# Performance work log

Measured on AMD Instinct MI355X. Metric: run time of the kernel, lower is better.

## Reference

```python
import jax, jax.numpy as jnp
import numpy as np

ROPE_BASE = 10000.0
NEG_INF = jnp.finfo(jnp.float32).min


def _rope(x, pos):
    # x: [B, L, H, D], pos: [L] absolute positions. Rotate-half RoPE.
    D = x.shape[-1]
    half = D // 2
    inv_freq = 1.0 / (ROPE_BASE ** (jnp.arange(half, dtype=jnp.float32) / half))
    ang = pos.astype(jnp.float32)[:, None] * inv_freq  # [L, half]
    cos = jnp.cos(ang)[None, :, None, :]
    sin = jnp.sin(ang)[None, :, None, :]
    x1, x2 = x[..., :half], x[..., half:]
    return jnp.concatenate([x1 * cos - x2 * sin, x1 * sin + x2 * cos], axis=-1)


def setup_inputs() -> dict:
    key = jax.random.key(0)
    kq, kk, kv = jax.random.split(key, 3)
    B, L, H, Dh = 4, 4096, 16, 64
    return {
        "q": jax.random.normal(kq, (B, L, H, Dh), dtype=jnp.float32),
        "k": jax.random.normal(kk, (B, L, H, Dh), dtype=jnp.float32),
        "v": jax.random.normal(kv, (B, L, H, Dh), dtype=jnp.float32),
        "chunk_size": 1024,
        "start_index": 0,
    }


def reference(q, k, v, chunk_size, start_index):
    B, L, H, Dh = q.shape
    Dv = v.shape[-1]
    C = chunk_size
    assert L % C == 0  # chosen shapes avoid padding; original pads otherwise
    n = L // C
    # Per-chunk RoPE with offset start_index + chunk_offset equals
    # full-sequence RoPE at absolute positions start_index + arange(L).
    pos = start_index + jnp.arange(L)
    q_rot = _rope(q.astype(jnp.float32), pos)
    k_rot = _rope(k.astype(jnp.float32), pos)
    qc = q_rot.reshape(B, n, C, H, Dh)
    kc = k_rot.reshape(B, n, C, H, Dh)
    vc = v.astype(jnp.float32).reshape(B, n, C, H, Dv)
    # Unscaled (scale=1.0) block-diagonal causal attention.
    scores = jnp.einsum("bnqhd,bnkhd->bnhqk", qc, kc)
    causal = jnp.tril(jnp.ones((C, C), dtype=jnp.bool_))
    scores = jnp.where(causal, scores, NEG_INF)
    attn = jax.nn.softmax(scores, axis=-1)
    attn = jnp.where(jnp.isnan(attn), 0.0, attn)
    out = jnp.einsum("bnhqk,bnkhd->bnqhd", attn, vc)
    return out.reshape(B, L, H, Dv).astype(q.dtype)
```

## Files before the change

kernel.cpp:

```cpp
#include <hip/hip_runtime.h>

typedef _Float16 f16x8 __attribute__((ext_vector_type(8)));
typedef _Float16 f16x4 __attribute__((ext_vector_type(4)));
typedef _Float16 f16x2 __attribute__((ext_vector_type(2)));
typedef float    f32x4 __attribute__((ext_vector_type(4)));

#define B_N    4
#define L_TOT  4096
#define H_N    16
#define DH     64
#define HALF_D 32
#define QT     64
#define KT     64
#define LDSP   72

#define LOG2_BASE 13.287712379549449f
#define LOG2E     1.4426950408889634f

#define TAB_BYTES  ((size_t)L_TOT * 64 * sizeof(float))
#define IMG_BYTES  ((size_t)B_N * H_N * 64 * 8192)

__global__ void rope_table_kernel(const int* __restrict__ sidx, float* __restrict__ tab) {
    int idx = blockIdx.x * 256 + (int)threadIdx.x;
    if (idx >= L_TOT * HALF_D) return;
    int l = idx >> 5;
    int j = idx & 31;
    float invf = exp2f(-(float)j * (LOG2_BASE / (float)HALF_D));
    float ang = (float)(sidx[0] + l) * invf;
    float s, c;
    sincosf(ang, &s, &c);
    tab[l * 64 + j] = c;
    tab[l * 64 + HALF_D + j] = s;
}

__global__ __launch_bounds__(256)
void prep_kernel(const float* __restrict__ k, const float* __restrict__ v,
                 const float* __restrict__ tab,
                 unsigned char* __restrict__ kimg, unsigned char* __restrict__ vimg)
{
    __shared__ float Vs[64][65];
    int bid = (int)blockIdx.x;
    int t = (int)threadIdx.x;

    if (bid < 4096) {
        int task = bid * 256 + t;
        int c = task & 3;
        int rowid = task >> 2;
        int l = rowid & (L_TOT - 1);
        int bh = rowid >> 12;
        int b = bh >> 4, h = bh & 15;
        int d0 = c * 8;
        const float* src = k + (((size_t)b * L_TOT + l) * H_N + h) * (size_t)DH;
        f32x4 x1a = *(const f32x4*)(src + d0);
        f32x4 x1b = *(const f32x4*)(src + d0 + 4);
        f32x4 x2a = *(const f32x4*)(src + d0 + HALF_D);
        f32x4 x2b = *(const f32x4*)(src + d0 + HALF_D + 4);
        const float* tr = tab + (size_t)l * 64 + d0;
        f32x4 ca = *(const f32x4*)(tr);
        f32x4 cb = *(const f32x4*)(tr + 4);
        f32x4 sa = *(const f32x4*)(tr + HALF_D);
        f32x4 sb = *(const f32x4*)(tr + HALF_D + 4);
        f16x8 olo, ohi;
#pragma unroll
        for (int j = 0; j < 4; ++j) {
            olo[j]     = (_Float16)(x1a[j] * ca[j] - x2a[j] * sa[j]);
            olo[j + 4] = (_Float16)(x1b[j] * cb[j] - x2b[j] * sb[j]);
            ohi[j]     = (_Float16)(x1a[j] * sa[j] + x2a[j] * ca[j]);
            ohi[j + 4] = (_Float16)(x1b[j] * sb[j] + x2b[j] * cb[j]);
        }
        size_t tile = (size_t)bh * 64 + (l >> 6);
        unsigned char* dst = kimg + tile * 8192 + (size_t)(l & 63) * 128;
        int sw = (c ^ (l & 7)) << 4;
        *(f16x8*)(dst + sw)        = olo;
        *(f16x8*)(dst + (sw ^ 64)) = ohi;
    } else {
        int vb = bid - 4096;
        int tile = vb & 63;
        int h = (vb >> 6) & 15;
        int b = vb >> 10;
        int kbase = tile * 64;
        int row = t >> 2, cb = t & 3;
        const float* src = v + (((size_t)b * L_TOT + kbase + row) * H_N + h) * (size_t)DH + cb * 16;
        f32x4 a0 = *(const f32x4*)(src);
        f32x4 a1 = *(const f32x4*)(src + 4);
        f32x4 a2 = *(const f32x4*)(src + 8);
        f32x4 a3 = *(const f32x4*)(src + 12);
#pragma unroll
        for (int j = 0; j < 4; ++j) {
            Vs[row][cb * 16 + j]      = a0[j];
            Vs[row][cb * 16 + 4 + j]  = a1[j];
            Vs[row][cb * 16 + 8 + j]  = a2[j];
            Vs[row][cb * 16 + 12 + j] = a3[j];
        }
        __syncthreads();
        size_t tbase = ((size_t)(b * 16 + h) * 64 + tile) * 8192;
#pragma unroll
        for (int e = 0; e < 2; ++e) {
            int task = e * 256 + t;
            int dv = task >> 3, c = task & 7;
            f16x8 o;
#pragma unroll
            for (int j = 0; j < 8; ++j) o[j] = (_Float16)Vs[8 * c + j][dv];
            *(f16x8*)(vimg + tbase + (size_t)dv * 128 + ((c ^ (dv & 7)) << 4)) = o;
        }
    }
}

__device__ __forceinline__ void gl_lds16(const void* g, void* lds) {
    __builtin_amdgcn_global_load_lds(
        (const __attribute__((address_space(1))) unsigned int*)g,
        (__attribute__((address_space(3))) unsigned int*)lds, 16, 0, 0);
}

__global__ __launch_bounds__(256, 4)
void attn_main_kernel(const float* __restrict__ q, const int* __restrict__ csz,
                      const float* __restrict__ tab,
                      const unsigned char* __restrict__ kimg,
                      const unsigned char* __restrict__ vimg,
                      float* __restrict__ out) {
    __shared__ __align__(16) unsigned char smem[40960];

    const int tid  = (int)threadIdx.x;
    const int lane = tid & 63;
    const int w    = tid >> 6;
    const int cl   = lane & 15;
    const int g    = lane >> 4;
    const int e7   = cl & 7;

    const int bid0  = (int)blockIdx.x;
    const int wg    = (bid0 & 7) * 512 + (bid0 >> 3);
    const int qx    = wg & 63;
    const int h     = (wg >> 6) & 15;
    const int b     = wg >> 10;

    const int C   = csz[0];
    const int tpc = C >> 6;
    const int qtile = qx ^ ((tpc - 1) & 63);
    const int kb0 = (qtile / tpc) * tpc;

    const int qr = qtile * QT + w * 16 + cl;
    const float* qs = q + (((size_t)b * L_TOT + qr) * H_N + h) * (size_t)DH;
    f32x4 x1a = *(const f32x4*)(qs + 8 * g);
    f32x4 x1b = *(const f32x4*)(qs + 8 * g + 4);
    f32x4 x2a = *(const f32x4*)(qs + 8 * g + HALF_D);
    f32x4 x2b = *(const f32x4*)(qs + 8 * g + HALF_D + 4);
    const float* tr = tab + (size_t)qr * 64 + 8 * g;
    f32x4 ca = *(const f32x4*)(tr);
    f32x4 cb = *(const f32x4*)(tr + 4);
    f32x4 sa = *(const f32x4*)(tr + HALF_D);
    f32x4 sb = *(const f32x4*)(tr + HALF_D + 4);
    f16x8 qa0, qa1;
#pragma unroll
    for (int j = 0; j < 4; ++j) {
        qa0[j]     = (_Float16)((x1a[j] * ca[j] - x2a[j] * sa[j]) * LOG2E);
        qa0[j + 4] = (_Float16)((x1b[j] * cb[j] - x2b[j] * sb[j]) * LOG2E);
        qa1[j]     = (_Float16)((x1a[j] * sa[j] + x2a[j] * ca[j]) * LOG2E);
        qa1[j + 4] = (_Float16)((x1b[j] * sb[j] + x2b[j] * cb[j]) * LOG2E);
    }

    const unsigned char* ksrc = kimg + (size_t)(b * 16 + h) * 64 * 8192;
    const unsigned char* vsrc = vimg + (size_t)(b * 16 + h) * 64 * 8192;

    const int krd = cl * 128 + ((g ^ e7) << 4);
    const int pwb = cl * 128 + (((g >> 1) ^ e7) << 4) + (g & 1) * 8;
    char* Pw = (char*)(smem + 32768 + w * 2048);

    f32x4 o[4] = {};
    float m = -3e38f, l = 0.f;

    {
        const unsigned char* gk = ksrc + (size_t)kb0 * 8192;
        const unsigned char* gv = vsrc + (size_t)kb0 * 8192;
        gl_lds16(gk + tid * 16,        smem + tid * 16);
        gl_lds16(gk + tid * 16 + 4096, smem + tid * 16 + 4096);
        gl_lds16(gv + tid * 16,        smem + 16384 + tid * 16);
        gl_lds16(gv + tid * 16 + 4096, smem + 16384 + tid * 16 + 4096);
    }

    int pb = 0;
    for (int kb = kb0; kb <= qtile; ++kb) {
        __syncthreads();

        const char* Kb = (const char*)(smem + pb * 8192);
        const char* Vb = (const char*)(smem + 16384 + pb * 8192);
        if (kb < qtile) {
            const unsigned char* nk = ksrc + (size_t)(kb + 1) * 8192;
            const unsigned char* nv = vsrc + (size_t)(kb + 1) * 8192;
            unsigned char* lk = smem + (pb ^ 1) * 8192;
            unsigned char* lv = smem + 16384 + (pb ^ 1) * 8192;
            gl_lds16(nk + tid * 16,        lk + tid * 16);
            gl_lds16(nk + tid * 16 + 4096, lk + tid * 16 + 4096);
            gl_lds16(nv + tid * 16,        lv + tid * 16);
            gl_lds16(nv + tid * 16 + 4096, lv + tid * 16 + 4096);
        }

        f32x4 sc[4];
        __builtin_amdgcn_s_setprio(1);
#pragma unroll
        for (int ct = 0; ct < 4; ++ct) {
            f16x8 kf0 = *(const f16x8*)(Kb + krd + ct * 2048);
            f16x8 kf1 = *(const f16x8*)(Kb + ((krd + ct * 2048) ^ 64));
            f32x4 z = {};
            z = __builtin_amdgcn_mfma_f32_16x16x32_f16(kf0, qa0, z, 0, 0, 0);
            sc[ct] = __builtin_amdgcn_mfma_f32_16x16x32_f16(kf1, qa1, z, 0, 0, 0);
        }
        __builtin_amdgcn_s_setprio(0);

        if (kb == qtile) {
            const int qloc = w * 16 + cl;
#pragma unroll
            for (int ct = 0; ct < 4; ++ct)
#pragma unroll
                for (int r = 0; r < 4; ++r)
                    if (ct * 16 + 4 * g + r > qloc) sc[ct][r] = -3e38f;
        }

        float mx = sc[0][0];
#pragma unroll
        for (int ct = 0; ct < 4; ++ct)
#pragma unroll
            for (int r = 0; r < 4; ++r) mx = fmaxf(mx, sc[ct][r]);
        mx = fmaxf(mx, __shfl_xor(mx, 16));
        mx = fmaxf(mx, __shfl_xor(mx, 32));
        if (__any(mx - m > 8.0f)) {
            float mn  = fmaxf(m, mx);
            float scl = exp2f(m - mn);
            m = mn;
            l *= scl;
#pragma unroll
            for (int ct = 0; ct < 4; ++ct)
#pragma unroll
                for (int r = 0; r < 4; ++r) o[ct][r] *= scl;
        }
        float ps = 0.f;
#pragma unroll
        for (int ct = 0; ct < 4; ++ct)
#pragma unroll
            for (int r = 0; r < 4; ++r) {
                float p = exp2f(sc[ct][r] - m);
                sc[ct][r] = p;
                ps += p;
            }
        ps += __shfl_xor(ps, 16);
        ps += __shfl_xor(ps, 32);
        l += ps;

#pragma unroll
        for (int c = 0; c < 4; ++c) {
            f16x2 lo = __builtin_bit_cast(f16x2, __builtin_amdgcn_cvt_pkrtz(sc[c][0], sc[c][1]));
            f16x2 hi = __builtin_bit_cast(f16x2, __builtin_amdgcn_cvt_pkrtz(sc[c][2], sc[c][3]));
            f16x4 pv = __builtin_shufflevector(lo, hi, 0, 1, 2, 3);
            *(f16x4*)(Pw + (pwb ^ (c << 5))) = pv;
        }

        f16x8 pa0 = *(const f16x8*)(Pw + krd);
        f16x8 pa1 = *(const f16x8*)(Pw + (krd ^ 64));
        __builtin_amdgcn_s_setprio(1);
#pragma unroll
        for (int ct = 0; ct < 4; ++ct) {
            f16x8 v0 = *(const f16x8*)(Vb + krd + ct * 2048);
            o[ct] = __builtin_amdgcn_mfma_f32_16x16x32_f16(v0, pa0, o[ct], 0, 0, 0);
        }
#pragma unroll
        for (int ct = 0; ct < 4; ++ct) {
            f16x8 v1 = *(const f16x8*)(Vb + ((krd + ct * 2048) ^ 64));
            o[ct] = __builtin_amdgcn_mfma_f32_16x16x32_f16(v1, pa1, o[ct], 0, 0, 0);
        }
        __builtin_amdgcn_s_setprio(0);

        pb ^= 1;
    }

    __syncthreads();
    float* Ow = (float*)smem;
    float inv = 1.f / l;
#pragma unroll
    for (int ct = 0; ct < 4; ++ct)
#pragma unroll
        for (int r = 0; r < 4; ++r)
            Ow[(w * 16 + cl) * 66 + ct * 16 + 4 * g + r] = o[ct][r] * inv;
    __syncthreads();
    int row_l = tid >> 2;
    int cb4 = (tid & 3) * 16;
    const float* orow = Ow + row_l * 66 + cb4;
    float* gdst = out + (((size_t)b * L_TOT + qtile * QT + row_l) * H_N + h) * (size_t)DH + cb4;
#pragma unroll
    for (int jj = 0; jj < 4; ++jj) {
        f32x4 val;
#pragma unroll
        for (int x = 0; x < 4; ++x) val[x] = orow[4 * jj + x];
        *(f32x4*)(gdst + 4 * jj) = val;
    }
}

__device__ __forceinline__ void rope_cs_inline(float pos, int d, float* cc, float* ss) {
    float invf = exp2f(-(float)d * (LOG2_BASE / (float)HALF_D));
    float s, c;
    sincosf(pos * invf, &s, &c);
    *cc = c;
    *ss = s;
}

template<bool TAB>
__global__ __launch_bounds__(256)
void chunked_attn_kernel(const float* __restrict__ q, const float* __restrict__ k,
                         const float* __restrict__ v, const int* __restrict__ csz,
                         const int* __restrict__ sidx, const float* __restrict__ tab,
                         float* __restrict__ out)
{
    __shared__ _Float16 Ks[KT][LDSP];
    __shared__ _Float16 Vt[DH][LDSP];
    __shared__ _Float16 Ps[4][16][LDSP];

    const int tid  = (int)threadIdx.x;
    const int lane = tid & 63;
    const int w    = tid >> 6;
    const int cl   = lane & 15;
    const int g    = lane >> 4;

    const int bid   = (int)blockIdx.x;
    const int qtile = bid & (L_TOT / QT - 1);
    const int h     = (bid >> 6) & (H_N - 1);
    const int b     = bid >> 10;

    const int C   = csz[0];
    const int S0  = sidx[0];
    const int tpc = C / KT;
    const int kb0 = (qtile / tpc) * tpc;

    const int qrow = qtile * QT + w * 16 + cl;
    const size_t qoff = (((size_t)b * L_TOT + qrow) * H_N + h) * (size_t)DH;
    f32x4 x1a = *(const f32x4*)(q + qoff + 8 * g);
    f32x4 x1b = *(const f32x4*)(q + qoff + 8 * g + 4);
    f32x4 x2a = *(const f32x4*)(q + qoff + 8 * g + HALF_D);
    f32x4 x2b = *(const f32x4*)(q + qoff + 8 * g + HALF_D + 4);
    f32x4 ca, cb, sa, sb;
    if (TAB) {
        const float* tr = tab + (size_t)qrow * 64 + 8 * g;
        ca = *(const f32x4*)(tr);
        cb = *(const f32x4*)(tr + 4);
        sa = *(const f32x4*)(tr + HALF_D);
        sb = *(const f32x4*)(tr + HALF_D + 4);
    } else {
        float pos = (float)(S0 + qrow);
#pragma unroll
        for (int j = 0; j < 4; ++j) {
            float c0, s0, c1, s1;
            rope_cs_inline(pos, 8 * g + j,     &c0, &s0);
            rope_cs_inline(pos, 8 * g + 4 + j, &c1, &s1);
            ca[j] = c0; sa[j] = s0;
            cb[j] = c1; sb[j] = s1;
        }
    }
    f16x8 qa0, qa1;
#pragma unroll
    for (int j = 0; j < 4; ++j) {
        qa0[j]     = (_Float16)(x1a[j] * ca[j] - x2a[j] * sa[j]);
        qa0[j + 4] = (_Float16)(x1b[j] * cb[j] - x2b[j] * sb[j]);
        qa1[j]     = (_Float16)(x1a[j] * sa[j] + x2a[j] * ca[j]);
        qa1[j + 4] = (_Float16)(x1b[j] * sb[j] + x2b[j] * cb[j]);
    }

    f32x4 o[4] = {};
    float m_r[4], l_r[4];
#pragma unroll
    for (int r = 0; r < 4; ++r) { m_r[r] = -3e38f; l_r[r] = 0.f; }

    for (int kb = kb0; kb <= qtile; ++kb) {
        __syncthreads();
        const int kbase = kb * KT;

#pragma unroll
        for (int e = 0; e < 2; ++e) {
            int task = e * 256 + tid;
            int kk = task >> 3;
            int dg = (task & 7) * 4;
            int grow = kbase + kk;
            size_t off = (((size_t)b * L_TOT + grow) * H_N + h) * (size_t)DH;
            f32x4 x1 = *(const f32x4*)(k + off + dg);
            f32x4 x2 = *(const f32x4*)(k + off + dg + HALF_D);
            f32x4 cc, ss;
            if (TAB) {
                const float* tr2 = tab + (size_t)grow * 64 + dg;
                cc = *(const f32x4*)(tr2);
                ss = *(const f32x4*)(tr2 + HALF_D);
            } else {
                float pos = (float)(S0 + grow);
#pragma unroll
                for (int j = 0; j < 4; ++j) {
                    float c0, s0;
                    rope_cs_inline(pos, dg + j, &c0, &s0);
                    cc[j] = c0; ss[j] = s0;
                }
            }
            f16x4 o1, o2;
#pragma unroll
            for (int j = 0; j < 4; ++j) {
                o1[j] = (_Float16)(x1[j] * cc[j] - x2[j] * ss[j]);
                o2[j] = (_Float16)(x1[j] * ss[j] + x2[j] * cc[j]);
            }
            *(f16x4*)&Ks[kk][dg]          = o1;
            *(f16x4*)&Ks[kk][dg + HALF_D] = o2;
        }

#pragma unroll
        for (int e = 0; e < 4; ++e) {
            int task = e * 256 + tid;
            int kk = task >> 4;
            int dq = (task & 15) * 4;
            int grow = kbase + kk;
            size_t off = (((size_t)b * L_TOT + grow) * H_N + h) * (size_t)DH + dq;
            f32x4 x = *(const f32x4*)(v + off);
#pragma unroll
            for (int i = 0; i < 4; ++i) Vt[dq + i][kk] = (_Float16)x[i];
        }
        __syncthreads();

        f32x4 sc[4];
#pragma unroll
        for (int ct = 0; ct < 4; ++ct) {
            f16x8 kf0 = *(const f16x8*)&Ks[ct * 16 + cl][8 * g];
            f16x8 kf1 = *(const f16x8*)&Ks[ct * 16 + cl][8 * g + HALF_D];
            f32x4 z = {};
            z = __builtin_amdgcn_mfma_f32_16x16x32_f16(qa0, kf0, z, 0, 0, 0);
            sc[ct] = __builtin_amdgcn_mfma_f32_16x16x32_f16(qa1, kf1, z, 0, 0, 0);
        }

        const int rowt = w * 16 + 4 * g;
        if (kb == qtile) {
#pragma unroll
            for (int ct = 0; ct < 4; ++ct)
#pragma unroll
                for (int r = 0; r < 4; ++r)
                    if (ct * 16 + cl > rowt + r) sc[ct][r] = -3e38f;
        }

        f32x4 mt;
#pragma unroll
        for (int r = 0; r < 4; ++r)
            mt[r] = fmaxf(fmaxf(sc[0][r], sc[1][r]), fmaxf(sc[2][r], sc[3][r]));
#pragma unroll
        for (int off = 1; off < 16; off <<= 1) {
#pragma unroll
            for (int r = 0; r < 4; ++r)
                mt[r] = fmaxf(mt[r], __shfl_xor(mt[r], off));
        }
        float scale_r[4];
#pragma unroll
        for (int r = 0; r < 4; ++r) {
            float mn = fmaxf(m_r[r], mt[r]);
            scale_r[r] = __expf(m_r[r] - mn);
            m_r[r] = mn;
        }
        f32x4 psum = {};
#pragma unroll
        for (int ct = 0; ct < 4; ++ct) {
#pragma unroll
            for (int r = 0; r < 4; ++r) {
                float p = __expf(sc[ct][r] - m_r[r]);
                sc[ct][r] = p;
                psum[r] += p;
            }
        }
#pragma unroll
        for (int off = 1; off < 16; off <<= 1) {
#pragma unroll
            for (int r = 0; r < 4; ++r)
                psum[r] += __shfl_xor(psum[r], off);
        }
#pragma unroll
        for (int r = 0; r < 4; ++r) l_r[r] = l_r[r] * scale_r[r] + psum[r];
#pragma unroll
        for (int ct = 0; ct < 4; ++ct)
#pragma unroll
            for (int r = 0; r < 4; ++r) o[ct][r] *= scale_r[r];

#pragma unroll
        for (int ct = 0; ct < 4; ++ct)
#pragma unroll
            for (int r = 0; r < 4; ++r)
                Ps[w][4 * g + r][ct * 16 + cl] = (_Float16)sc[ct][r];

#pragma unroll
        for (int st = 0; st < 2; ++st) {
            f16x8 pa = *(const f16x8*)&Ps[w][cl][8 * g + 32 * st];
#pragma unroll
            for (int ct = 0; ct < 4; ++ct) {
                f16x8 vb = *(const f16x8*)&Vt[ct * 16 + cl][8 * g + 32 * st];
                o[ct] = __builtin_amdgcn_mfma_f32_16x16x32_f16(pa, vb, o[ct], 0, 0, 0);
            }
        }
    }

#pragma unroll
    for (int ct = 0; ct < 4; ++ct) {
#pragma unroll
        for (int r = 0; r < 4; ++r) {
            int row = qtile * QT + w * 16 + 4 * g + r;
            float val = o[ct][r] / l_r[r];
            out[(((size_t)b * L_TOT + row) * H_N + h) * (size_t)DH + ct * 16 + cl] = val;
        }
    }
}

extern "C" void kernel_launch(void* const* d_in, const int* in_sizes, int n_in,
                              void* d_out, int out_size, void* d_ws, size_t ws_size,
                              hipStream_t stream) {
    const float* q  = (const float*)d_in[0];
    const float* k  = (const float*)d_in[1];
    const float* v  = (const float*)d_in[2];
    const int* csz  = (const int*)d_in[3];
    const int* sidx = (const int*)d_in[4];
    float* out = (float*)d_out;

    const size_t TOTAL = TAB_BYTES + 2 * IMG_BYTES;
    const int grid = B_N * H_N * (L_TOT / QT);

    if (ws_size >= TOTAL) {
        float* tab = (float*)d_ws;
        unsigned char* kimg = (unsigned char*)d_ws + TAB_BYTES;
        unsigned char* vimg = kimg + IMG_BYTES;
        rope_table_kernel<<<(L_TOT * HALF_D + 255) / 256, 256, 0, stream>>>(sidx, tab);
        prep_kernel<<<8192, 256, 0, stream>>>(k, v, tab, kimg, vimg);
        attn_main_kernel<<<grid, 256, 0, stream>>>(q, csz, tab, kimg, vimg, out);
    } else if (ws_size >= TAB_BYTES) {
        float* tab = (float*)d_ws;
        rope_table_kernel<<<(L_TOT * HALF_D + 255) / 256, 256, 0, stream>>>(sidx, tab);
        chunked_attn_kernel<true><<<grid, 256, 0, stream>>>(q, k, v, csz, sidx, tab, out);
    } else {
        chunked_attn_kernel<false><<<grid, 256, 0, stream>>>(q, k, v, csz, sidx, nullptr, out);
    }
}
```

Measured before the change: 149.7 us.

## Read K/V fragments directly from global memory instead of LDS double-buffering

Drops the LDS double-buffered staging of K and V tiles (global_load_lds plus per-iteration barriers). Each wave now loads its MFMA fragments straight from the prepacked global images, and the XOR swizzle is removed from both the packing kernel and the readers. Shared memory shrinks to the P scratch and output staging, and launch bounds rise to 5 blocks per CU to raise occupancy. The cost is that each of the four waves fetches the same K/V tile from global/L2 separately, and there is no explicit prefetch overlap.

```diff
diff --git a/kernel.cpp b/kernel.cpp
--- a/kernel.cpp
+++ b/kernel.cpp
@@ -70,9 +70,8 @@
         }
         size_t tile = (size_t)bh * 64 + (l >> 6);
         unsigned char* dst = kimg + tile * 8192 + (size_t)(l & 63) * 128;
-        int sw = (c ^ (l & 7)) << 4;
-        *(f16x8*)(dst + sw)        = olo;
-        *(f16x8*)(dst + (sw ^ 64)) = ohi;
+        *(f16x8*)(dst + (c << 4))      = olo;
+        *(f16x8*)(dst + (c << 4) + 64) = ohi;
     } else {
         int vb = bid - 4096;
         int tile = vb & 63;
@@ -101,24 +100,18 @@
             f16x8 o;
 #pragma unroll
             for (int j = 0; j < 8; ++j) o[j] = (_Float16)Vs[8 * c + j][dv];
-            *(f16x8*)(vimg + tbase + (size_t)dv * 128 + ((c ^ (dv & 7)) << 4)) = o;
+            *(f16x8*)(vimg + tbase + (size_t)dv * 128 + (c << 4)) = o;
         }
     }
 }
 
-__device__ __forceinline__ void gl_lds16(const void* g, void* lds) {
-    __builtin_amdgcn_global_load_lds(
-        (const __attribute__((address_space(1))) unsigned int*)g,
-        (__attribute__((address_space(3))) unsigned int*)lds, 16, 0, 0);
-}
-
-__global__ __launch_bounds__(256, 4)
+__global__ __launch_bounds__(256, 5)
 void attn_main_kernel(const float* __restrict__ q, const int* __restrict__ csz,
                       const float* __restrict__ tab,
                       const unsigned char* __restrict__ kimg,
                       const unsigned char* __restrict__ vimg,
                       float* __restrict__ out) {
-    __shared__ __align__(16) unsigned char smem[40960];
+    __shared__ __align__(16) unsigned char smem[16896];
 
     const int tid  = (int)threadIdx.x;
     const int lane = tid & 63;
@@ -161,45 +154,24 @@
     const unsigned char* ksrc = kimg + (size_t)(b * 16 + h) * 64 * 8192;
     const unsigned char* vsrc = vimg + (size_t)(b * 16 + h) * 64 * 8192;
 
+    const int rln = cl * 128 + g * 16;
     const int krd = cl * 128 + ((g ^ e7) << 4);
     const int pwb = cl * 128 + (((g >> 1) ^ e7) << 4) + (g & 1) * 8;
-    char* Pw = (char*)(smem + 32768 + w * 2048);
+    char* Pw = (char*)(smem + w * 2048);
 
     f32x4 o[4] = {};
     float m = -3e38f, l = 0.f;
 
-    {
-        const unsigned char* gk = ksrc + (size_t)kb0 * 8192;
-        const unsigned char* gv = vsrc + (size_t)kb0 * 8192;
-        gl_lds16(gk + tid * 16,        smem + tid * 16);
-        gl_lds16(gk + tid * 16 + 4096, smem + tid * 16 + 4096);
-        gl_lds16(gv + tid * 16,        smem + 16384 + tid * 16);
-        gl_lds16(gv + tid * 16 + 4096, smem + 16384 + tid * 16 + 4096);
-    }
-
-    int pb = 0;
     for (int kb = kb0; kb <= qtile; ++kb) {
-        __syncthreads();
-
-        const char* Kb = (const char*)(smem + pb * 8192);
-        const char* Vb = (const char*)(smem + 16384 + pb * 8192);
-        if (kb < qtile) {
-            const unsigned char* nk = ksrc + (size_t)(kb + 1) * 8192;
-            const unsigned char* nv = vsrc + (size_t)(kb + 1) * 8192;
-            unsigned char* lk = smem + (pb ^ 1) * 8192;
-            unsigned char* lv = smem + 16384 + (pb ^ 1) * 8192;
-            gl_lds16(nk + tid * 16,        lk + tid * 16);
-            gl_lds16(nk + tid * 16 + 4096, lk + tid * 16 + 4096);
-            gl_lds16(nv + tid * 16,        lv + tid * 16);
-            gl_lds16(nv + tid * 16 + 4096, lv + tid * 16 + 4096);
-        }
+        const char* kt = (const char*)(ksrc + (size_t)kb * 8192);
+        const char* vt = (const char*)(vsrc + (size_t)kb * 8192);
 
         f32x4 sc[4];
         __builtin_amdgcn_s_setprio(1);
 #pragma unroll
         for (int ct = 0; ct < 4; ++ct) {
-            f16x8 kf0 = *(const f16x8*)(Kb + krd + ct * 2048);
-            f16x8 kf1 = *(const f16x8*)(Kb + ((krd + ct * 2048) ^ 64));
+            f16x8 kf0 = *(const f16x8*)(kt + rln + ct * 2048);
+            f16x8 kf1 = *(const f16x8*)(kt + rln + ct * 2048 + 64);
             f32x4 z = {};
             z = __builtin_amdgcn_mfma_f32_16x16x32_f16(kf0, qa0, z, 0, 0, 0);
             sc[ct] = __builtin_amdgcn_mfma_f32_16x16x32_f16(kf1, qa1, z, 0, 0, 0);
@@ -258,17 +230,15 @@
         __builtin_amdgcn_s_setprio(1);
 #pragma unroll
         for (int ct = 0; ct < 4; ++ct) {
-            f16x8 v0 = *(const f16x8*)(Vb + krd + ct * 2048);
+            f16x8 v0 = *(const f16x8*)(vt + rln + ct * 2048);
             o[ct] = __builtin_amdgcn_mfma_f32_16x16x32_f16(v0, pa0, o[ct], 0, 0, 0);
         }
 #pragma unroll
         for (int ct = 0; ct < 4; ++ct) {
-            f16x8 v1 = *(const f16x8*)(Vb + ((krd + ct * 2048) ^ 64));
+            f16x8 v1 = *(const f16x8*)(vt + rln + ct * 2048 + 64);
             o[ct] = __builtin_amdgcn_mfma_f32_16x16x32_f16(v1, pa1, o[ct], 0, 0, 0);
         }
         __builtin_amdgcn_s_setprio(0);
-
-        pb ^= 1;
     }
 
     __syncthreads();
```

After: 389.8 us. +160.4%, slower.

## Switch attention kernel to 32x32 MFMA with register-resident P and 2-wave blocks

Applied to the files above, without the earlier changes.

Rewrites the main attention kernel so each wave owns 32 query rows and uses 32x32x16 MFMA for both QK^T and PV. The softmax probabilities are packed to f16 and swapped between half-waves with lane shuffles instead of a round trip through LDS. The block shrinks to 128 threads, and outputs are written straight from registers without the LDS staging pass. This is meant to cut LDS traffic and instruction count per tile, at the cost of more accumulator registers and fewer waves per block to hide latency.

```diff
diff --git a/kernel.cpp b/kernel.cpp
--- a/kernel.cpp
+++ b/kernel.cpp
@@ -2,8 +2,8 @@
 
 typedef _Float16 f16x8 __attribute__((ext_vector_type(8)));
 typedef _Float16 f16x4 __attribute__((ext_vector_type(4)));
-typedef _Float16 f16x2 __attribute__((ext_vector_type(2)));
 typedef float    f32x4 __attribute__((ext_vector_type(4)));
+typedef float    f32x16 __attribute__((ext_vector_type(16)));
 
 #define B_N    4
 #define L_TOT  4096
@@ -112,25 +112,29 @@
         (__attribute__((address_space(3))) unsigned int*)lds, 16, 0, 0);
 }
 
-__global__ __launch_bounds__(256, 4)
+__device__ __forceinline__ unsigned pku(float a, float b) {
+    return __builtin_bit_cast(unsigned, __builtin_amdgcn_cvt_pkrtz(a, b));
+}
+
+__global__ __launch_bounds__(128, 2)
 void attn_main_kernel(const float* __restrict__ q, const int* __restrict__ csz,
                       const float* __restrict__ tab,
                       const unsigned char* __restrict__ kimg,
                       const unsigned char* __restrict__ vimg,
                       float* __restrict__ out) {
-    __shared__ __align__(16) unsigned char smem[40960];
+    __shared__ __align__(16) unsigned char smem[32768];
 
     const int tid  = (int)threadIdx.x;
     const int lane = tid & 63;
     const int w    = tid >> 6;
-    const int cl   = lane & 15;
-    const int g    = lane >> 4;
-    const int e7   = cl & 7;
+    const int qi   = lane & 31;
+    const int h    = lane >> 5;
+    const int e7   = lane & 7;
 
     const int bid0  = (int)blockIdx.x;
     const int wg    = (bid0 & 7) * 512 + (bid0 >> 3);
     const int qx    = wg & 63;
-    const int h     = (wg >> 6) & 15;
+    const int hh    = (wg >> 6) & 15;
     const int b     = wg >> 10;
 
     const int C   = csz[0];
@@ -138,43 +142,49 @@
     const int qtile = qx ^ ((tpc - 1) & 63);
     const int kb0 = (qtile / tpc) * tpc;
 
-    const int qr = qtile * QT + w * 16 + cl;
-    const float* qs = q + (((size_t)b * L_TOT + qr) * H_N + h) * (size_t)DH;
-    f32x4 x1a = *(const f32x4*)(qs + 8 * g);
-    f32x4 x1b = *(const f32x4*)(qs + 8 * g + 4);
-    f32x4 x2a = *(const f32x4*)(qs + 8 * g + HALF_D);
-    f32x4 x2b = *(const f32x4*)(qs + 8 * g + HALF_D + 4);
-    const float* tr = tab + (size_t)qr * 64 + 8 * g;
-    f32x4 ca = *(const f32x4*)(tr);
-    f32x4 cb = *(const f32x4*)(tr + 4);
-    f32x4 sa = *(const f32x4*)(tr + HALF_D);
-    f32x4 sb = *(const f32x4*)(tr + HALF_D + 4);
-    f16x8 qa0, qa1;
+    const int qg = qtile * QT + 32 * w + qi;
+    const int qloc = 32 * w + qi;
+
+    const float* qs = q + (((size_t)b * L_TOT + qg) * H_N + hh) * (size_t)DH;
+    const int d0 = 8 * h;
+    f32x4 xa0 = *(const f32x4*)(qs + d0);       f32x4 xa1 = *(const f32x4*)(qs + d0 + 4);
+    f32x4 xb0 = *(const f32x4*)(qs + d0 + 16);  f32x4 xb1 = *(const f32x4*)(qs + d0 + 20);
+    f32x4 xc0 = *(const f32x4*)(qs + d0 + 32);  f32x4 xc1 = *(const f32x4*)(qs + d0 + 36);
+    f32x4 xd0 = *(const f32x4*)(qs + d0 + 48);  f32x4 xd1 = *(const f32x4*)(qs + d0 + 52);
+    const float* tr = tab + (size_t)qg * 64;
+    f32x4 ca0 = *(const f32x4*)(tr + d0);       f32x4 ca1 = *(const f32x4*)(tr + d0 + 4);
+    f32x4 cb0 = *(const f32x4*)(tr + d0 + 16);  f32x4 cb1 = *(const f32x4*)(tr + d0 + 20);
+    f32x4 sa0 = *(const f32x4*)(tr + 32 + d0);      f32x4 sa1 = *(const f32x4*)(tr + 32 + d0 + 4);
+    f32x4 sb0 = *(const f32x4*)(tr + 32 + d0 + 16); f32x4 sb1 = *(const f32x4*)(tr + 32 + d0 + 20);
+    f16x8 qf0, qf1, qf2, qf3;
 #pragma unroll
     for (int j = 0; j < 4; ++j) {
-        qa0[j]     = (_Float16)((x1a[j] * ca[j] - x2a[j] * sa[j]) * LOG2E);
-        qa0[j + 4] = (_Float16)((x1b[j] * cb[j] - x2b[j] * sb[j]) * LOG2E);
-        qa1[j]     = (_Float16)((x1a[j] * sa[j] + x2a[j] * ca[j]) * LOG2E);
-        qa1[j + 4] = (_Float16)((x1b[j] * sb[j] + x2b[j] * cb[j]) * LOG2E);
-    }
-
-    const unsigned char* ksrc = kimg + (size_t)(b * 16 + h) * 64 * 8192;
-    const unsigned char* vsrc = vimg + (size_t)(b * 16 + h) * 64 * 8192;
-
-    const int krd = cl * 128 + ((g ^ e7) << 4);
-    const int pwb = cl * 128 + (((g >> 1) ^ e7) << 4) + (g & 1) * 8;
-    char* Pw = (char*)(smem + 32768 + w * 2048);
-
-    f32x4 o[4] = {};
+        qf0[j]     = (_Float16)((xa0[j] * ca0[j] - xc0[j] * sa0[j]) * LOG2E);
+        qf0[j + 4] = (_Float16)((xa1[j] * ca1[j] - xc1[j] * sa1[j]) * LOG2E);
+        qf1[j]     = (_Float16)((xb0[j] * cb0[j] - xd0[j] * sb0[j]) * LOG2E);
+        qf1[j + 4] = (_Float16)((xb1[j] * cb1[j] - xd1[j] * sb1[j]) * LOG2E);
+        qf2[j]     = (_Float16)((xa0[j] * sa0[j] + xc0[j] * ca0[j]) * LOG2E);
+        qf2[j + 4] = (_Float16)((xa1[j] * sa1[j] + xc1[j] * ca1[j]) * LOG2E);
+        qf3[j]     = (_Float16)((xb0[j] * sb0[j] + xd0[j] * cb0[j]) * LOG2E);
+        qf3[j + 4] = (_Float16)((xb1[j] * sb1[j] + xd1[j] * cb1[j]) * LOG2E);
+    }
+
+    const unsigned char* ksrc = kimg + (size_t)(b * 16 + hh) * 64 * 8192;
+    const unsigned char* vsrc = vimg + (size_t)(b * 16 + hh) * 64 * 8192;
+
+    const int rbase = qi * 128;
+
+    f32x16 acc0 = {}, acc1 = {};
     float m = -3e38f, l = 0.f;
 
     {
         const unsigned char* gk = ksrc + (size_t)kb0 * 8192;
         const unsigned char* gv = vsrc + (size_t)kb0 * 8192;
-        gl_lds16(gk + tid * 16,        smem + tid * 16);
-        gl_lds16(gk + tid * 16 + 4096, smem + tid * 16 + 4096);
-        gl_lds16(gv + tid * 16,        smem + 16384 + tid * 16);
-        gl_lds16(gv + tid * 16 + 4096, smem + 16384 + tid * 16 + 4096);
+#pragma unroll
+        for (int e = 0; e < 4; ++e) {
+            gl_lds16(gk + tid * 16 + e * 2048, smem + tid * 16 + e * 2048);
+            gl_lds16(gv + tid * 16 + e * 2048, smem + 16384 + tid * 16 + e * 2048);
+        }
     }
 
     int pb = 0;
@@ -188,39 +198,50 @@
             const unsigned char* nv = vsrc + (size_t)(kb + 1) * 8192;
             unsigned char* lk = smem + (pb ^ 1) * 8192;
             unsigned char* lv = smem + 16384 + (pb ^ 1) * 8192;
-            gl_lds16(nk + tid * 16,        lk + tid * 16);
-            gl_lds16(nk + tid * 16 + 4096, lk + tid * 16 + 4096);
-            gl_lds16(nv + tid * 16,        lv + tid * 16);
-            gl_lds16(nv + tid * 16 + 4096, lv + tid * 16 + 4096);
-        }
-
-        f32x4 sc[4];
+#pragma unroll
+            for (int e = 0; e < 4; ++e) {
+                gl_lds16(nk + tid * 16 + e * 2048, lk + tid * 16 + e * 2048);
+                gl_lds16(nv + tid * 16 + e * 2048, lv + tid * 16 + e * 2048);
+            }
+        }
+
+        f32x16 sc0 = {}, sc1 = {};
         __builtin_amdgcn_s_setprio(1);
 #pragma unroll
-        for (int ct = 0; ct < 4; ++ct) {
-            f16x8 kf0 = *(const f16x8*)(Kb + krd + ct * 2048);
-            f16x8 kf1 = *(const f16x8*)(Kb + ((krd + ct * 2048) ^ 64));
-            f32x4 z = {};
-            z = __builtin_amdgcn_mfma_f32_16x16x32_f16(kf0, qa0, z, 0, 0, 0);
-            sc[ct] = __builtin_amdgcn_mfma_f32_16x16x32_f16(kf1, qa1, z, 0, 0, 0);
+        for (int s = 0; s < 4; ++s) {
+            f16x8 kf = *(const f16x8*)(Kb + rbase + (((h + 2 * s) ^ e7) << 4));
+            const f16x8 qv = (s == 0) ? qf0 : (s == 1) ? qf1 : (s == 2) ? qf2 : qf3;
+            sc0 = __builtin_amdgcn_mfma_f32_32x32x16_f16(kf, qv, sc0, 0, 0, 0);
+        }
+#pragma unroll
+        for (int s = 0; s < 4; ++s) {
+            f16x8 kf = *(const f16x8*)(Kb + 4096 + rbase + (((h + 2 * s) ^ e7) << 4));
+            const f16x8 qv = (s == 0) ? qf0 : (s == 1) ? qf1 : (s == 2) ? qf2 : qf3;
+            sc1 = __builtin_amdgcn_mfma_f32_32x32x16_f16(kf, qv, sc1, 0, 0, 0);
         }
         __builtin_amdgcn_s_setprio(0);
 
         if (kb == qtile) {
-            const int qloc = w * 16 + cl;
-#pragma unroll
-            for (int ct = 0; ct < 4; ++ct)
-#pragma unroll
-                for (int r = 0; r < 4; ++r)
-                    if (ct * 16 + 4 * g + r > qloc) sc[ct][r] = -3e38f;
-        }
-
-        float mx = sc[0][0];
-#pragma unroll
-        for (int ct = 0; ct < 4; ++ct)
-#pragma unroll
-            for (int r = 0; r < 4; ++r) mx = fmaxf(mx, sc[ct][r]);
-        mx = fmaxf(mx, __shfl_xor(mx, 16));
+#pragma unroll
+            for (int r = 0; r < 16; ++r) {
+                const int kl = (r & 3) + 8 * (r >> 2) + 4 * h;
+                if (kl > qloc)      sc0[r] = -3e38f;
+                if (kl + 32 > qloc) sc1[r] = -3e38f;
+            }
+        }
+
+        float m0 = sc0[0], m1 = sc0[1], m2 = sc0[2], m3 = sc0[3];
+#pragma unroll
+        for (int r = 4; r < 16; r += 4) {
+            m0 = fmaxf(m0, sc0[r]);     m1 = fmaxf(m1, sc0[r + 1]);
+            m2 = fmaxf(m2, sc0[r + 2]); m3 = fmaxf(m3, sc0[r + 3]);
+        }
+#pragma unroll
+        for (int r = 0; r < 16; r += 4) {
+            m0 = fmaxf(m0, sc1[r]);     m1 = fmaxf(m1, sc1[r + 1]);
+            m2 = fmaxf(m2, sc1[r + 2]); m3 = fmaxf(m3, sc1[r + 3]);
+        }
+        float mx = fmaxf(fmaxf(m0, m1), fmaxf(m2, m3));
         mx = fmaxf(mx, __shfl_xor(mx, 32));
         if (__any(mx - m > 8.0f)) {
             float mn  = fmaxf(m, mx);
@@ -228,68 +249,70 @@
             m = mn;
             l *= scl;
 #pragma unroll
-            for (int ct = 0; ct < 4; ++ct)
-#pragma unroll
-                for (int r = 0; r < 4; ++r) o[ct][r] *= scl;
-        }
-        float ps = 0.f;
-#pragma unroll
-        for (int ct = 0; ct < 4; ++ct)
-#pragma unroll
-            for (int r = 0; r < 4; ++r) {
-                float p = exp2f(sc[ct][r] - m);
-                sc[ct][r] = p;
-                ps += p;
-            }
-        ps += __shfl_xor(ps, 16);
+            for (int r = 0; r < 16; ++r) { acc0[r] *= scl; acc1[r] *= scl; }
+        }
+        unsigned pkA[8], pkB[8];
+        float s0 = 0.f, s1 = 0.f, s2 = 0.f, s3 = 0.f;
+#pragma unroll
+        for (int i = 0; i < 8; ++i) {
+            float a0 = exp2f(sc0[2 * i] - m);
+            float a1 = exp2f(sc0[2 * i + 1] - m);
+            s0 += a0; s1 += a1;
+            pkA[i] = pku(a0, a1);
+            float b0 = exp2f(sc1[2 * i] - m);
+            float b1 = exp2f(sc1[2 * i + 1] - m);
+            s2 += b0; s3 += b1;
+            pkB[i] = pku(b0, b1);
+        }
+        float ps = (s0 + s1) + (s2 + s3);
         ps += __shfl_xor(ps, 32);
         l += ps;
 
-#pragma unroll
-        for (int c = 0; c < 4; ++c) {
-            f16x2 lo = __builtin_bit_cast(f16x2, __builtin_amdgcn_cvt_pkrtz(sc[c][0], sc[c][1]));
-            f16x2 hi = __builtin_bit_cast(f16x2, __builtin_amdgcn_cvt_pkrtz(sc[c][2], sc[c][3]));
-            f16x4 pv = __builtin_shufflevector(lo, hi, 0, 1, 2, 3);
-            *(f16x4*)(Pw + (pwb ^ (c << 5))) = pv;
-        }
-
-        f16x8 pa0 = *(const f16x8*)(Pw + krd);
-        f16x8 pa1 = *(const f16x8*)(Pw + (krd ^ 64));
         __builtin_amdgcn_s_setprio(1);
 #pragma unroll
-        for (int ct = 0; ct < 4; ++ct) {
-            f16x8 v0 = *(const f16x8*)(Vb + krd + ct * 2048);
-            o[ct] = __builtin_amdgcn_mfma_f32_16x16x32_f16(v0, pa0, o[ct], 0, 0, 0);
-        }
-#pragma unroll
-        for (int ct = 0; ct < 4; ++ct) {
-            f16x8 v1 = *(const f16x8*)(Vb + ((krd + ct * 2048) ^ 64));
-            o[ct] = __builtin_amdgcn_mfma_f32_16x16x32_f16(v1, pa1, o[ct], 0, 0, 0);
+        for (int ks = 0; ks < 4; ++ks) {
+            const int base = 4 * (ks & 1);
+            unsigned w0, w1, w2, w3;
+            if (ks < 2) {
+                w0 = pkA[base];     w1 = pkA[base + 1];
+                w2 = pkA[base + 2]; w3 = pkA[base + 3];
+            } else {
+                w0 = pkB[base];     w1 = pkB[base + 1];
+                w2 = pkB[base + 2]; w3 = pkB[base + 3];
+            }
+            unsigned x = h ? w0 : w2;
+            unsigned y = h ? w1 : w3;
+            unsigned xs = (unsigned)__shfl_xor((int)x, 32);
+            unsigned ys = (unsigned)__shfl_xor((int)y, 32);
+            uint4 fw;
+            fw.x = h ? xs : w0;
+            fw.y = h ? ys : w1;
+            fw.z = h ? w2 : xs;
+            fw.w = h ? w3 : ys;
+            f16x8 pbf = __builtin_bit_cast(f16x8, fw);
+            const int voff = ((h + 2 * ks) ^ e7) << 4;
+            f16x8 v0 = *(const f16x8*)(Vb + rbase + voff);
+            f16x8 v1 = *(const f16x8*)(Vb + 4096 + rbase + voff);
+            acc0 = __builtin_amdgcn_mfma_f32_32x32x16_f16(v0, pbf, acc0, 0, 0, 0);
+            acc1 = __builtin_amdgcn_mfma_f32_32x32x16_f16(v1, pbf, acc1, 0, 0, 0);
         }
         __builtin_amdgcn_s_setprio(0);
 
         pb ^= 1;
     }
 
-    __syncthreads();
-    float* Ow = (float*)smem;
     float inv = 1.f / l;
-#pragma unroll
-    for (int ct = 0; ct < 4; ++ct)
-#pragma unroll
-        for (int r = 0; r < 4; ++r)
-            Ow[(w * 16 + cl) * 66 + ct * 16 + 4 * g + r] = o[ct][r] * inv;
-    __syncthreads();
-    int row_l = tid >> 2;
-    int cb4 = (tid & 3) * 16;
-    const float* orow = Ow + row_l * 66 + cb4;
-    float* gdst = out + (((size_t)b * L_TOT + qtile * QT + row_l) * H_N + h) * (size_t)DH + cb4;
-#pragma unroll
-    for (int jj = 0; jj < 4; ++jj) {
-        f32x4 val;
-#pragma unroll
-        for (int x = 0; x < 4; ++x) val[x] = orow[4 * jj + x];
-        *(f32x4*)(gdst + 4 * jj) = val;
+    float* orow = out + (((size_t)b * L_TOT + qg) * H_N + hh) * (size_t)DH;
+#pragma unroll
+    for (int t = 0; t < 4; ++t) {
+        f32x4 v0, v1;
+#pragma unroll
+        for (int u = 0; u < 4; ++u) {
+            v0[u] = acc0[4 * t + u] * inv;
+            v1[u] = acc1[4 * t + u] * inv;
+        }
+        *(f32x4*)(orow + 8 * t + 4 * h)      = v0;
+        *(f32x4*)(orow + 32 + 8 * t + 4 * h) = v1;
     }
 }
 
@@ -457,9 +480,9 @@
         for (int ct = 0; ct < 4; ++ct) {
 #pragma unroll
             for (int r = 0; r < 4; ++r) {
-                float p = __expf(sc[ct][r] - m_r[r]);
-                sc[ct][r] = p;
-                psum[r] += p;
+                float pz = __expf(sc[ct][r] - m_r[r]);
+                sc[ct][r] = pz;
+                psum[r] += pz;
             }
         }
 #pragma unroll
@@ -522,7 +545,7 @@
         unsigned char* vimg = kimg + IMG_BYTES;
         rope_table_kernel<<<(L_TOT * HALF_D + 255) / 256, 256, 0, stream>>>(sidx, tab);
         prep_kernel<<<8192, 256, 0, stream>>>(k, v, tab, kimg, vimg);
-        attn_main_kernel<<<grid, 256, 0, stream>>>(q, csz, tab, kimg, vimg, out);
+        attn_main_kernel<<<grid, 128, 0, stream>>>(q, csz, tab, kimg, vimg, out);
     } else if (ws_size >= TAB_BYTES) {
         float* tab = (float*)d_ws;
         rope_table_kernel<<<(L_TOT * HALF_D + 255) / 256, 256, 0, stream>>>(sidx, tab);
```

Measured after the change: 168.0 us. 1.12x slower.
